# Kernel tuning notes

Hardware: AMD Instinct MI355X
Metric: run time of the kernel (lower is better)

## Reference

```python
import jax, jax.numpy as jnp
import numpy as np

B, T, NIN = 128, 256, 16
H1 = H2 = 512
NACT = 4
SLOPE = 25.0  # snntorch FastSigmoid default slope

@jax.custom_vjp
def spike(x):
    return (x > 0).astype(x.dtype)

def _spike_fwd(x):
    return (x > 0).astype(x.dtype), x

def _spike_bwd(x, g):
    # FastSigmoid surrogate: d/dx = 1 / (slope*|x| + 1)^2
    return (g / (SLOPE * jnp.abs(x) + 1.0) ** 2,)

spike.defvjp(_spike_fwd, _spike_bwd)

def setup_inputs() -> dict:
    key = jax.random.key(0)
    ks = jax.random.split(key, 12)
    def lin(k, fan_in, shape):
        lim = 1.0 / np.sqrt(fan_in)
        return jax.random.uniform(k, shape, jnp.float32, -lim, lim)
    return {
        "batch": jax.random.uniform(ks[0], (B, T, NIN), jnp.float32, 0.0, 2.5),
        "W1": lin(ks[1], NIN, (H1, NIN)), "b1": lin(ks[2], NIN, (H1,)),
        "beta1": jax.random.uniform(ks[3], (H1,), jnp.float32),
        "thr1": jax.random.uniform(ks[4], (H1,), jnp.float32),
        "W2": lin(ks[5], H1, (H2, H1)), "b2": lin(ks[6], H1, (H2,)),
        "beta2": jax.random.uniform(ks[7], (H2,), jnp.float32),
        "thr2": jax.random.uniform(ks[8], (H2,), jnp.float32),
        "Wa": lin(ks[9], H2, (NACT, H2)), "ba": lin(ks[10], H2, (NACT,)),
        "beta_act": jnp.float32(0.95),
        "inp_min": jnp.float32(0.0),
        "inp_max": jnp.float32(2.5),
    }

def _lif_subtract(cur, mem, beta, thr):
    # snntorch Leaky: reset from PRE-update membrane, detached; subtract reset
    reset = jax.lax.stop_gradient((mem - thr > 0).astype(mem.dtype))
    mem = jnp.clip(beta, 0.0, 1.0) * mem + cur - reset * thr
    return spike(mem - thr), mem

def reference(batch, W1, b1, beta1, thr1, W2, b2, beta2, thr2, Wa, ba, beta_act, inp_min, inp_max):
    Bb = batch.shape[0]
    x_seq = jnp.swapaxes(batch, 0, 1)  # [T, B, NIN]
    mem1 = jnp.zeros((Bb, W1.shape[0]), batch.dtype)
    mem2 = jnp.zeros((Bb, W2.shape[0]), batch.dtype)
    mem_a = jnp.zeros((Bb, Wa.shape[0]), batch.dtype)

    def step(carry, x):
        mem1, mem2, mem_a = carry
        x = (x - inp_min) / (inp_max - inp_min)
        spk1, mem1 = _lif_subtract(x @ W1.T + b1, mem1, beta1, thr1)
        spk2, mem2 = _lif_subtract(spk1 @ W2.T + b2, mem2, beta2, thr2)
        act = spk2 @ Wa.T + ba
        # action_lif: reset_mechanism='none', beta=0.95 learnable
        mem_a = jnp.clip(beta_act, 0.0, 1.0) * mem_a + act
        return (mem1, mem2, mem_a), mem_a.reshape(-1)  # torch: mem_act.reshape((1,-1))

    _, vals = jax.lax.scan(step, (mem1, mem2, mem_a), x_seq)
    # torch.stack(values, dim=1) of (1, B*NACT) tensors -> (1, T, B*NACT)
    return vals[None, :, :]
```

## Files before the change

### kernel.cpp

```cpp
#include <hip/hip_runtime.h>
#include <stdint.h>

typedef __attribute__((ext_vector_type(8))) short short8;
typedef __attribute__((ext_vector_type(4))) float f32x4;

#define T_STEPS 256
#define BATCH   128

#define LDS_BARRIER() asm volatile("s_waitcnt lgkmcnt(0)\n\ts_barrier" ::: "memory")

static __device__ inline unsigned short f2bf(float f) {
    unsigned int u = __float_as_uint(f);
    unsigned int r = u + 0x7FFFu + ((u >> 16) & 1u);
    return (unsigned short)(r >> 16);
}
static __device__ inline unsigned pack_hi16(unsigned a, unsigned b) {
    return __builtin_amdgcn_perm(b, a, 0x07060302u);
}
static __device__ inline void gload_lds16(const unsigned short* g, unsigned short* l) {
    __builtin_amdgcn_global_load_lds(
        (const __attribute__((address_space(1))) unsigned int*)(const void*)g,
        (__attribute__((address_space(3))) unsigned int*)(void*)l,
        16, 0, 0);
}

__global__ __launch_bounds__(256) void k_prep(
    const float* __restrict__ W2, const float* __restrict__ W1,
    const float* __restrict__ b1, const float* __restrict__ thr1,
    const float* __restrict__ imin_p, const float* __restrict__ imax_p,
    const float* __restrict__ batch,
    unsigned short* __restrict__ W2hi, unsigned short* __restrict__ W2lo,
    unsigned short* __restrict__ W1rows, float* __restrict__ b1s,
    unsigned short* __restrict__ Xf)
{
    int blk = blockIdx.x, tid = threadIdx.x;
    if (blk < 256) {
        int gid = blk * 256 + tid;
        f32x4 wv = *(const f32x4*)(W2 + (size_t)gid * 4);
        unsigned short hi[4], lo[4];
#pragma unroll
        for (int e = 0; e < 4; ++e) {
            float wf = wv[e];
            unsigned short h = f2bf(wf);
            float hf = __uint_as_float(((unsigned int)h) << 16);
            hi[e] = h;
            lo[e] = f2bf(wf - hf);
        }
        uint2 ph, pl;
        ph.x = (unsigned)hi[0] | ((unsigned)hi[1] << 16);
        ph.y = (unsigned)hi[2] | ((unsigned)hi[3] << 16);
        pl.x = (unsigned)lo[0] | ((unsigned)lo[1] << 16);
        pl.y = (unsigned)lo[2] | ((unsigned)lo[3] << 16);
        *(uint2*)(W2hi + (size_t)gid * 4) = ph;
        *(uint2*)(W2lo + (size_t)gid * 4) = pl;
    } else if (blk < 258) {
        int h = (blk - 256) * 256 + tid;
        float wsc = 1.0f / thr1[h];
        unsigned short row[64];
#pragma unroll
        for (int k = 0; k < 16; ++k) {
            float wv = W1[h * 16 + k] * wsc;
            unsigned a = __float_as_uint(wv) & 0xFFFF0000u;
            float r1 = wv - __uint_as_float(a);
            unsigned m = __float_as_uint(r1) & 0xFFFF0000u;
            float r2 = r1 - __uint_as_float(m);
            unsigned l = __float_as_uint(r2) & 0xFFFF0000u;
            row[k]      = (unsigned short)(a >> 16);
            row[16 + k] = (unsigned short)(m >> 16);
            row[32 + k] = (unsigned short)(l >> 16);
            row[48 + k] = 0;
        }
        b1s[h] = b1[h] * wsc;
        uint4* dst = (uint4*)(W1rows + (size_t)h * 64);
#pragma unroll
        for (int i = 0; i < 8; ++i) dst[i] = ((uint4*)row)[i];
    } else {
        int gid    = (blk - 258) * 256 + tid;
        int lane32 = gid & 31;
        int btile  = (gid >> 5) & 7;
        int t      = gid >> 8;
        int q1 = lane32 >> 4, m15 = lane32 & 15;
        int b  = btile * 16 + m15;
        float imin = imin_p[0];
        float isc  = 1.0f / (imax_p[0] - imin);
        const float* xp = batch + ((size_t)b * T_STEPS + t) * 16 + q1 * 8;
        unsigned uh[8], um[8], ul[8];
#pragma unroll
        for (int j = 0; j < 8; ++j) {
            float xv = (xp[j] - imin) * isc;
            unsigned a = __float_as_uint(xv) & 0xFFFF0000u;
            float r1 = xv - __uint_as_float(a);
            unsigned m = __float_as_uint(r1) & 0xFFFF0000u;
            float r2 = r1 - __uint_as_float(m);
            unsigned l = __float_as_uint(r2) & 0xFFFF0000u;
            uh[j] = a; um[j] = m; ul[j] = l;
        }
        uint4 XH, XM, XL;
        XH.x = pack_hi16(uh[0], uh[1]); XH.y = pack_hi16(uh[2], uh[3]);
        XH.z = pack_hi16(uh[4], uh[5]); XH.w = pack_hi16(uh[6], uh[7]);
        XM.x = pack_hi16(um[0], um[1]); XM.y = pack_hi16(um[2], um[3]);
        XM.z = pack_hi16(um[4], um[5]); XM.w = pack_hi16(um[6], um[7]);
        XL.x = pack_hi16(ul[0], ul[1]); XL.y = pack_hi16(ul[2], ul[3]);
        XL.z = pack_hi16(ul[4], ul[5]); XL.w = pack_hi16(ul[6], ul[7]);
        unsigned short* dst = Xf + ((size_t)t * 8 + btile) * 1024 + lane32 * 8;
        *(uint4*)(dst +   0) = XH;
        *(uint4*)(dst + 256) = XM;
        *(uint4*)(dst + 512) = XL;
    }
}

union XF { uint4 u; short8 s; };

__global__ __launch_bounds__(1024, 4) void k_main(
    const unsigned short* __restrict__ Xf,
    const unsigned short* __restrict__ W2hi, const unsigned short* __restrict__ W2lo,
    const unsigned short* __restrict__ W1rows, const float* __restrict__ b1s,
    const float* __restrict__ beta1, const float* __restrict__ b2,
    const float* __restrict__ beta2, const float* __restrict__ thr2,
    unsigned short* __restrict__ spkbits)
{
    __shared__ unsigned short Aw[8192];
    __shared__ float Cbuf[2][4096];
    __shared__ unsigned short Xs[4096];

    int tid  = threadIdx.x;
    int lane = tid & 63;
    int w    = tid >> 6;
    int q = lane >> 4, m15 = lane & 15;
    int btile = blockIdx.x & 7;
    int slice = blockIdx.x >> 3;

    short8 A1[2], A2[2], A3[2];
#pragma unroll
    for (int c = 0; c < 2; ++c) {
        const unsigned short* rp = W1rows + (size_t)(w * 32 + c * 16 + m15) * 64;
        A1[c] = *(const short8*)(rp + q * 8);
        A2[c] = *(const short8*)(rp + q * 8 + (q >> 1) * 16);
        A3[c] = *(const short8*)(rp + 16 + q * 8);
    }
    int jg = slice * 16 + m15;
    short8 bhi = *(const short8*)(W2hi + (size_t)jg * 512 + w * 32 + q * 8);
    short8 blo = *(const short8*)(W2lo + (size_t)jg * 512 + w * 32 + q * 8);

    f32x4 b14[2], bet1[2];
#pragma unroll
    for (int c = 0; c < 2; ++c) {
        int h0 = w * 32 + c * 16 + q * 4;
        b14[c] = *(const f32x4*)(b1s + h0);
        f32x4 bb = *(const f32x4*)(beta1 + h0);
#pragma unroll
        for (int r = 0; r < 4; ++r) bet1[c][r] = fminf(fmaxf(bb[r], 0.0f), 1.0f);
    }
    float m1[8], spk1f[8];
#pragma unroll
    for (int i = 0; i < 8; ++i) { m1[i] = 0.0f; spk1f[i] = 0.0f; }

    float beta2r = fminf(fmaxf(beta2[jg], 0.0f), 1.0f);
    float thr2r  = thr2[jg];
    float nthr2  = -thr2r;
    float b2r    = b2[jg];
    float m2 = 0.0f, spk2f = 0.0f;

    const unsigned short* xgbase = Xf + (size_t)btile * 1024 + (size_t)lane * 8;
    int l31x8 = (lane & 31) * 8;
    int o1 = l31x8;
    int o2 = l31x8 + 256;
    int o3 = l31x8 + (lane < 32 ? 512 : 0);
    int o4 = l31x8 + (lane < 32 ? 512 : 256);

    unsigned short* myAw = Aw + w * 512;
    int wr0 = (0 * 2 + (q >> 1)) * 128 + (m15 ^ (q >> 1)) * 8 + (q & 1) * 4;
    int wr1 = (1 * 2 + (q >> 1)) * 128 + (m15 ^ (q >> 1)) * 8 + (q & 1) * 4;
    int rdo = (q * 16 + (m15 ^ (q & 1))) * 8;

    if (w == 15) {
        gload_lds16(xgbase,              Xs);
        gload_lds16(xgbase + 512,        Xs + 512);
        gload_lds16(xgbase + 8192,       Xs + 1024);
        gload_lds16(xgbase + 8192 + 512, Xs + 1536);
        asm volatile("s_waitcnt vmcnt(0)" ::: "memory");
    }
    __syncthreads();

    XF xc[4], xn[4];
    {
        const unsigned short* s = Xs;
        xc[0].u = *(const uint4*)(s + o1);
        xc[1].u = *(const uint4*)(s + o2);
        xc[2].u = *(const uint4*)(s + o3);
        xc[3].u = *(const uint4*)(s + o4);
    }

    auto body = [&](int ts, XF* xcur, XF* xnx) __attribute__((always_inline)) {
        int buf = ts & 1;
        if (w == 15) {
            int t2 = (ts + 2 < T_STEPS) ? ts + 2 : T_STEPS - 1;
            const unsigned short* g = xgbase + (size_t)t2 * 8192;
            unsigned short* l = Xs + (((ts + 2) & 3) << 10);
            gload_lds16(g,       l);
            gload_lds16(g + 512, l + 512);
        }
        {
            const unsigned short* s = Xs + (((ts + 1) & 3) << 10);
            xnx[0].u = *(const uint4*)(s + o1);
            xnx[1].u = *(const uint4*)(s + o2);
            xnx[2].u = *(const uint4*)(s + o3);
            xnx[3].u = *(const uint4*)(s + o4);
        }

        f32x4 D[2];
#pragma unroll
        for (int c = 0; c < 2; ++c) {
            D[c] = __builtin_amdgcn_mfma_f32_16x16x32_bf16(A1[c], xcur[0].s, b14[c], 0, 0, 0);
            D[c] = __builtin_amdgcn_mfma_f32_16x16x32_bf16(A1[c], xcur[1].s, D[c], 0, 0, 0);
            D[c] = __builtin_amdgcn_mfma_f32_16x16x32_bf16(A2[c], xcur[2].s, D[c], 0, 0, 0);
            D[c] = __builtin_amdgcn_mfma_f32_16x16x32_bf16(A3[c], xcur[3].s, D[c], 0, 0, 0);
        }
#pragma unroll
        for (int i = 0; i < 8; ++i) {
            int c = i >> 2, r = i & 3;
            float mv = fmaf(bet1[c][r], m1[i], D[c][r]);
            mv -= spk1f[i];
            bool sp = mv > 1.0f;
            m1[i] = mv;
            spk1f[i] = sp ? 1.0f : 0.0f;
        }
        {
            uint2 pk0, pk1;
            pk0.x = pack_hi16(__float_as_uint(spk1f[0]), __float_as_uint(spk1f[1]));
            pk0.y = pack_hi16(__float_as_uint(spk1f[2]), __float_as_uint(spk1f[3]));
            pk1.x = pack_hi16(__float_as_uint(spk1f[4]), __float_as_uint(spk1f[5]));
            pk1.y = pack_hi16(__float_as_uint(spk1f[6]), __float_as_uint(spk1f[7]));
            *(uint2*)(myAw + wr0) = pk0;
            *(uint2*)(myAw + wr1) = pk1;
        }
        union { uint4 u; short8 s; } af;
        af.u = *(uint4*)(myAw + rdo);
        f32x4 C2 = { 0.f, 0.f, 0.f, 0.f };
        C2 = __builtin_amdgcn_mfma_f32_16x16x32_bf16(af.s, bhi, C2, 0, 0, 0);
        C2 = __builtin_amdgcn_mfma_f32_16x16x32_bf16(af.s, blo, C2, 0, 0, 0);
#pragma unroll
        for (int r = 0; r < 4; ++r)
            Cbuf[buf][r * 1024 + w * 64 + lane] = C2[r];
        if (w == 15) asm volatile("s_waitcnt vmcnt(0)" ::: "memory");
        LDS_BARRIER();
        if (w < 4) {
            float cur2 = b2r;
#pragma unroll
            for (int wp = 0; wp < 16; ++wp) cur2 += Cbuf[buf][w * 1024 + wp * 64 + lane];
            m2 = fmaf(beta2r, m2, cur2);
            m2 = fmaf(spk2f, nthr2, m2);
            bool sp2 = m2 > thr2r;
            spk2f = sp2 ? 1.0f : 0.0f;
            unsigned long long mask = __ballot(sp2);
            if (lane < 4) {
                unsigned short v = (unsigned short)(mask >> (lane * 16));
                spkbits[((size_t)ts * BATCH + btile * 16 + lane * 4 + w) * 32 + slice] = v;
            }
        }
    };

#pragma unroll 1
    for (int ts = 0; ts < T_STEPS; ts += 2) {
        body(ts, xc, xn);
        body(ts + 1, xn, xc);
    }
}

__global__ __launch_bounds__(256) void k_act(
    const unsigned short* __restrict__ spkbits,
    const float* __restrict__ Wa, const float* __restrict__ ba,
    const float* __restrict__ beta_act_p, float* __restrict__ out)
{
    __shared__ f32x4 waT[512];
    __shared__ f32x4 sc[256];
    int tid = threadIdx.x;
    int b   = blockIdx.x;

    for (int j = tid; j < 512; j += 256) {
        f32x4 v = { Wa[j], Wa[512 + j], Wa[1024 + j], Wa[1536 + j] };
        waT[j] = v;
    }
    float bact = fminf(fmaxf(beta_act_p[0], 0.0f), 1.0f);
    f32x4 acc = { ba[0], ba[1], ba[2], ba[3] };
    __syncthreads();

    const unsigned short* sp = spkbits + ((size_t)tid * BATCH + b) * 32;
    unsigned int wbuf[16];
#pragma unroll
    for (int r = 0; r < 4; ++r) {
        uint4 v = *(const uint4*)(sp + r * 8);
        wbuf[r*4+0] = v.x; wbuf[r*4+1] = v.y; wbuf[r*4+2] = v.z; wbuf[r*4+3] = v.w;
    }
    for (int s = 0; s < 32; ++s) {
        unsigned int wd = (wbuf[s >> 1] >> ((s & 1) * 16)) & 0xFFFFu;
#pragma unroll
        for (int i = 0; i < 16; ++i) {
            float sel = ((wd >> i) & 1u) ? 1.0f : 0.0f;
            f32x4 wv = waT[s * 16 + i];
            acc[0] = fmaf(sel, wv[0], acc[0]);
            acc[1] = fmaf(sel, wv[1], acc[1]);
            acc[2] = fmaf(sel, wv[2], acc[2]);
            acc[3] = fmaf(sel, wv[3], acc[3]);
        }
    }
    sc[tid] = acc;
    __syncthreads();
    float bd = bact;
    for (int d = 1; d < 256; d <<= 1) {
        f32x4 cv = sc[tid];
        f32x4 pv = { 0.f, 0.f, 0.f, 0.f };
        if (tid >= d) pv = sc[tid - d];
        __syncthreads();
        cv[0] = fmaf(bd, pv[0], cv[0]);
        cv[1] = fmaf(bd, pv[1], cv[1]);
        cv[2] = fmaf(bd, pv[2], cv[2]);
        cv[3] = fmaf(bd, pv[3], cv[3]);
        sc[tid] = cv;
        __syncthreads();
        bd *= bd;
    }
    f32x4 res = sc[tid];
    *(f32x4*)(out + (size_t)tid * 512 + b * 4) = res;
}

extern "C" void kernel_launch(void* const* d_in, const int* in_sizes, int n_in,
                              void* d_out, int out_size, void* d_ws, size_t ws_size,
                              hipStream_t stream)
{
    const float* batch    = (const float*)d_in[0];
    const float* W1       = (const float*)d_in[1];
    const float* b1       = (const float*)d_in[2];
    const float* beta1    = (const float*)d_in[3];
    const float* thr1     = (const float*)d_in[4];
    const float* W2       = (const float*)d_in[5];
    const float* b2       = (const float*)d_in[6];
    const float* beta2    = (const float*)d_in[7];
    const float* thr2     = (const float*)d_in[8];
    const float* Wa       = (const float*)d_in[9];
    const float* ba       = (const float*)d_in[10];
    const float* beta_act = (const float*)d_in[11];
    const float* inp_min  = (const float*)d_in[12];
    const float* inp_max  = (const float*)d_in[13];
    float* out            = (float*)d_out;

    char* ws = (char*)d_ws;
    unsigned short* W2hi    = (unsigned short*)ws;
    unsigned short* W2lo    = (unsigned short*)(ws + (512u << 10));
    unsigned short* W1rows  = (unsigned short*)(ws + (1u << 20));
    float*          b1s     = (float*)(ws + (1u << 20) + (64u << 10));
    unsigned short* Xf      = (unsigned short*)(ws + (2u << 20));
    unsigned short* spkbits = (unsigned short*)(ws + (10u << 20));

    hipLaunchKernelGGL(k_prep, dim3(514), dim3(256), 0, stream,
                       W2, W1, b1, thr1, inp_min, inp_max, batch,
                       W2hi, W2lo, W1rows, b1s, Xf);
    hipLaunchKernelGGL(k_main, dim3(256), dim3(1024), 0, stream,
                       Xf, W2hi, W2lo, W1rows, b1s, beta1, b2, beta2, thr2, spkbits);
    hipLaunchKernelGGL(k_act, dim3(128), dim3(256), 0, stream, spkbits, Wa, ba, beta_act, out);
}
```

Before: 289.0 us.

## Halve per-step barriers by batching layer-2 reductions and split action scan

```diff
diff --git a/kernel.cpp b/kernel.cpp
--- a/kernel.cpp
+++ b/kernel.cpp
@@ -120,8 +120,8 @@
     unsigned short* __restrict__ spkbits)
 {
     __shared__ unsigned short Aw[8192];
-    __shared__ float Cbuf[2][4096];
-    __shared__ unsigned short Xs[4096];
+    __shared__ float Cbuf[4][4096];
+    __shared__ unsigned short Xs[8192];
 
     int tid  = threadIdx.x;
     int lane = tid & 63;
@@ -174,10 +174,11 @@
     int rdo = (q * 16 + (m15 ^ (q & 1))) * 8;
 
     if (w == 15) {
-        gload_lds16(xgbase,              Xs);
-        gload_lds16(xgbase + 512,        Xs + 512);
-        gload_lds16(xgbase + 8192,       Xs + 1024);
-        gload_lds16(xgbase + 8192 + 512, Xs + 1536);
+#pragma unroll
+        for (int s = 0; s < 4; ++s) {
+            gload_lds16(xgbase + (size_t)s * 8192,       Xs + s * 1024);
+            gload_lds16(xgbase + (size_t)s * 8192 + 512, Xs + s * 1024 + 512);
+        }
         asm volatile("s_waitcnt vmcnt(0)" ::: "memory");
     }
     __syncthreads();
@@ -191,23 +192,41 @@
         xc[3].u = *(const uint4*)(s + o4);
     }
 
-    auto body = [&](int ts, XF* xcur, XF* xnx) __attribute__((always_inline)) {
-        int buf = ts & 1;
-        if (w == 15) {
-            int t2 = (ts + 2 < T_STEPS) ? ts + 2 : T_STEPS - 1;
-            const unsigned short* g = xgbase + (size_t)t2 * 8192;
-            unsigned short* l = Xs + (((ts + 2) & 3) << 10);
-            gload_lds16(g,       l);
-            gload_lds16(g + 512, l + 512);
+    auto reduce_one = [&](int slot, int step) __attribute__((always_inline)) {
+        float cur2 = b2r;
+#pragma unroll
+        for (int wp = 0; wp < 16; ++wp) cur2 += Cbuf[slot][w * 1024 + wp * 64 + lane];
+        m2 = fmaf(beta2r, m2, cur2);
+        m2 = fmaf(spk2f, nthr2, m2);
+        bool sp2 = m2 > thr2r;
+        spk2f = sp2 ? 1.0f : 0.0f;
+        unsigned long long mask = __ballot(sp2);
+        if (lane < 4) {
+            unsigned short v = (unsigned short)(mask >> (lane * 16));
+            spkbits[((size_t)step * BATCH + btile * 16 + lane * 4 + w) * 32 + slice] = v;
+        }
+    };
+
+    auto gbody = [&](int ts, int k, XF* xcur, XF* xnx) __attribute__((always_inline)) {
+        if (((k & 1) == 0) && w == 15) {
+            int ta = ts + k + 4; if (ta > T_STEPS - 1) ta = T_STEPS - 1;
+            int tb = ts + k + 5; if (tb > T_STEPS - 1) tb = T_STEPS - 1;
+            const unsigned short* ga = xgbase + (size_t)ta * 8192;
+            const unsigned short* gb = xgbase + (size_t)tb * 8192;
+            unsigned short* la = Xs + ((k + 4) & 7) * 1024;
+            unsigned short* lb = Xs + ((k + 5) & 7) * 1024;
+            gload_lds16(ga,       la);
+            gload_lds16(ga + 512, la + 512);
+            gload_lds16(gb,       lb);
+            gload_lds16(gb + 512, lb + 512);
         }
         {
-            const unsigned short* s = Xs + (((ts + 1) & 3) << 10);
-            xnx[0].u = *(const uint4*)(s + o1);
-            xnx[1].u = *(const uint4*)(s + o2);
-            xnx[2].u = *(const uint4*)(s + o3);
-            xnx[3].u = *(const uint4*)(s + o4);
-        }
-
+            const unsigned short* sx = Xs + ((k + 1) & 7) * 1024;
+            xnx[0].u = *(const uint4*)(sx + o1);
+            xnx[1].u = *(const uint4*)(sx + o2);
+            xnx[2].u = *(const uint4*)(sx + o3);
+            xnx[3].u = *(const uint4*)(sx + o4);
+        }
         f32x4 D[2];
 #pragma unroll
         for (int c = 0; c < 2; ++c) {
@@ -239,89 +258,141 @@
         f32x4 C2 = { 0.f, 0.f, 0.f, 0.f };
         C2 = __builtin_amdgcn_mfma_f32_16x16x32_bf16(af.s, bhi, C2, 0, 0, 0);
         C2 = __builtin_amdgcn_mfma_f32_16x16x32_bf16(af.s, blo, C2, 0, 0, 0);
+        float* cb = Cbuf[k & 3];
 #pragma unroll
         for (int r = 0; r < 4; ++r)
-            Cbuf[buf][r * 1024 + w * 64 + lane] = C2[r];
-        if (w == 15) asm volatile("s_waitcnt vmcnt(0)" ::: "memory");
-        LDS_BARRIER();
-        if (w < 4) {
-            float cur2 = b2r;
-#pragma unroll
-            for (int wp = 0; wp < 16; ++wp) cur2 += Cbuf[buf][w * 1024 + wp * 64 + lane];
-            m2 = fmaf(beta2r, m2, cur2);
-            m2 = fmaf(spk2f, nthr2, m2);
-            bool sp2 = m2 > thr2r;
-            spk2f = sp2 ? 1.0f : 0.0f;
-            unsigned long long mask = __ballot(sp2);
-            if (lane < 4) {
-                unsigned short v = (unsigned short)(mask >> (lane * 16));
-                spkbits[((size_t)ts * BATCH + btile * 16 + lane * 4 + w) * 32 + slice] = v;
+            cb[r * 1024 + w * 64 + lane] = C2[r];
+        if (k & 1) {
+            if (w == 15) asm volatile("s_waitcnt vmcnt(0)" ::: "memory");
+            LDS_BARRIER();
+        }
+    };
+
+#pragma unroll 1
+    for (int ts = 0; ts < T_STEPS; ts += 8) {
+#pragma unroll
+        for (int kk = 0; kk < 4; ++kk) {
+            int k = kk * 2;
+            if (w < 4 && (ts + k >= 2)) {
+                reduce_one((k + 2) & 3, ts + k - 2);
+                reduce_one((k + 3) & 3, ts + k - 1);
             }
-        }
-    };
-
-#pragma unroll 1
-    for (int ts = 0; ts < T_STEPS; ts += 2) {
-        body(ts, xc, xn);
-        body(ts + 1, xn, xc);
-    }
-}
-
-__global__ __launch_bounds__(256) void k_act(
+            gbody(ts, k,     xc, xn);
+            gbody(ts, k + 1, xn, xc);
+        }
+    }
+    if (w < 4) {
+        reduce_one(2, T_STEPS - 2);
+        reduce_one(3, T_STEPS - 1);
+    }
+}
+
+__global__ __launch_bounds__(512) void k_act(
     const unsigned short* __restrict__ spkbits,
     const float* __restrict__ Wa, const float* __restrict__ ba,
+    const float* __restrict__ beta_act_p, float* __restrict__ out,
+    f32x4* __restrict__ Lws, f32x4* __restrict__ Cws)
+{
+    __shared__ f32x4 waT[512];
+    __shared__ f32x4 part[512];
+    __shared__ f32x4 sc[128];
+    int tid = threadIdx.x;
+    int b   = blockIdx.x & 127;
+    int c   = blockIdx.x >> 7;
+    int tl  = tid & 127;
+    int s   = tid >> 7;
+    int t   = c * 128 + tl;
+
+    {
+        f32x4 v = { Wa[tid], Wa[512 + tid], Wa[1024 + tid], Wa[1536 + tid] };
+        waT[tid] = v;
+    }
+    float bact = fminf(fmaxf(beta_act_p[0], 0.0f), 1.0f);
+    f32x4 acc;
+    if (s == 0) { acc[0] = ba[0]; acc[1] = ba[1]; acc[2] = ba[2]; acc[3] = ba[3]; }
+    else        { acc[0] = 0.f;   acc[1] = 0.f;   acc[2] = 0.f;   acc[3] = 0.f;   }
+    __syncthreads();
+
+    const unsigned short* sp = spkbits + ((size_t)t * BATCH + b) * 32 + s * 8;
+    uint4 v = *(const uint4*)sp;
+    unsigned int wbuf[4] = { v.x, v.y, v.z, v.w };
+#pragma unroll
+    for (int ww = 0; ww < 4; ++ww) {
+#pragma unroll
+        for (int half = 0; half < 2; ++half) {
+            unsigned int wd = (wbuf[ww] >> (half * 16)) & 0xFFFFu;
+            int seg = s * 8 + ww * 2 + half;
+#pragma unroll
+            for (int i = 0; i < 16; ++i) {
+                float sel = ((wd >> i) & 1u) ? 1.0f : 0.0f;
+                f32x4 wv = waT[seg * 16 + i];
+                acc[0] = fmaf(sel, wv[0], acc[0]);
+                acc[1] = fmaf(sel, wv[1], acc[1]);
+                acc[2] = fmaf(sel, wv[2], acc[2]);
+                acc[3] = fmaf(sel, wv[3], acc[3]);
+            }
+        }
+    }
+    part[tid] = acc;
+    __syncthreads();
+    if (tid < 128) {
+        f32x4 a0 = part[tid], a1 = part[tid + 128], a2 = part[tid + 256], a3 = part[tid + 384];
+        f32x4 sum;
+        sum[0] = ((a0[0] + a1[0]) + a2[0]) + a3[0];
+        sum[1] = ((a0[1] + a1[1]) + a2[1]) + a3[1];
+        sum[2] = ((a0[2] + a1[2]) + a2[2]) + a3[2];
+        sum[3] = ((a0[3] + a1[3]) + a2[3]) + a3[3];
+        sc[tid] = sum;
+    }
+    __syncthreads();
+    float bd = bact;
+    for (int d = 1; d < 128; d <<= 1) {
+        f32x4 cv = { 0.f, 0.f, 0.f, 0.f }, pv = { 0.f, 0.f, 0.f, 0.f };
+        if (tid < 128) {
+            cv = sc[tid];
+            if (tid >= d) pv = sc[tid - d];
+        }
+        __syncthreads();
+        if (tid < 128) {
+            cv[0] = fmaf(bd, pv[0], cv[0]);
+            cv[1] = fmaf(bd, pv[1], cv[1]);
+            cv[2] = fmaf(bd, pv[2], cv[2]);
+            cv[3] = fmaf(bd, pv[3], cv[3]);
+            sc[tid] = cv;
+        }
+        __syncthreads();
+        bd *= bd;
+    }
+    if (tid < 128) {
+        f32x4 res = sc[tid];
+        if (c == 0) {
+            *(f32x4*)(out + (size_t)t * 512 + b * 4) = res;
+            if (tl == 127) Cws[b] = res;
+        } else {
+            Lws[b * 128 + tl] = res;
+        }
+    }
+}
+
+__global__ __launch_bounds__(128) void k_act2(
+    const f32x4* __restrict__ Lws, const f32x4* __restrict__ Cws,
     const float* __restrict__ beta_act_p, float* __restrict__ out)
 {
-    __shared__ f32x4 waT[512];
-    __shared__ f32x4 sc[256];
-    int tid = threadIdx.x;
-    int b   = blockIdx.x;
-
-    for (int j = tid; j < 512; j += 256) {
-        f32x4 v = { Wa[j], Wa[512 + j], Wa[1024 + j], Wa[1536 + j] };
-        waT[j] = v;
-    }
+    int tl = threadIdx.x;
+    int b  = blockIdx.x;
     float bact = fminf(fmaxf(beta_act_p[0], 0.0f), 1.0f);
-    f32x4 acc = { ba[0], ba[1], ba[2], ba[3] };
-    __syncthreads();
-
-    const unsigned short* sp = spkbits + ((size_t)tid * BATCH + b) * 32;
-    unsigned int wbuf[16];
-#pragma unroll
-    for (int r = 0; r < 4; ++r) {
-        uint4 v = *(const uint4*)(sp + r * 8);
-        wbuf[r*4+0] = v.x; wbuf[r*4+1] = v.y; wbuf[r*4+2] = v.z; wbuf[r*4+3] = v.w;
-    }
-    for (int s = 0; s < 32; ++s) {
-        unsigned int wd = (wbuf[s >> 1] >> ((s & 1) * 16)) & 0xFFFFu;
-#pragma unroll
-        for (int i = 0; i < 16; ++i) {
-            float sel = ((wd >> i) & 1u) ? 1.0f : 0.0f;
-            f32x4 wv = waT[s * 16 + i];
-            acc[0] = fmaf(sel, wv[0], acc[0]);
-            acc[1] = fmaf(sel, wv[1], acc[1]);
-            acc[2] = fmaf(sel, wv[2], acc[2]);
-            acc[3] = fmaf(sel, wv[3], acc[3]);
-        }
-    }
-    sc[tid] = acc;
-    __syncthreads();
-    float bd = bact;
-    for (int d = 1; d < 256; d <<= 1) {
-        f32x4 cv = sc[tid];
-        f32x4 pv = { 0.f, 0.f, 0.f, 0.f };
-        if (tid >= d) pv = sc[tid - d];
-        __syncthreads();
-        cv[0] = fmaf(bd, pv[0], cv[0]);
-        cv[1] = fmaf(bd, pv[1], cv[1]);
-        cv[2] = fmaf(bd, pv[2], cv[2]);
-        cv[3] = fmaf(bd, pv[3], cv[3]);
-        sc[tid] = cv;
-        __syncthreads();
-        bd *= bd;
-    }
-    f32x4 res = sc[tid];
-    *(f32x4*)(out + (size_t)tid * 512 + b * 4) = res;
+    float p = 1.0f, base = bact;
+    int e = tl + 1;
+#pragma unroll
+    for (int i = 0; i < 8; ++i) { if (e & 1) p *= base; base *= base; e >>= 1; }
+    f32x4 L = Lws[b * 128 + tl];
+    f32x4 C = Cws[b];
+    f32x4 r;
+    r[0] = fmaf(p, C[0], L[0]);
+    r[1] = fmaf(p, C[1], L[1]);
+    r[2] = fmaf(p, C[2], L[2]);
+    r[3] = fmaf(p, C[3], L[3]);
+    *(f32x4*)(out + (size_t)(128 + tl) * 512 + b * 4) = r;
 }
 
 extern "C" void kernel_launch(void* const* d_in, const int* in_sizes, int n_in,
@@ -350,6 +421,8 @@
     unsigned short* W1rows  = (unsigned short*)(ws + (1u << 20));
     float*          b1s     = (float*)(ws + (1u << 20) + (64u << 10));
     unsigned short* Xf      = (unsigned short*)(ws + (2u << 20));
+    f32x4*          Lws     = (f32x4*)(ws + (6u << 20));
+    f32x4*          Cws     = (f32x4*)(ws + (6u << 20) + (256u << 10));
     unsigned short* spkbits = (unsigned short*)(ws + (10u << 20));
 
     hipLaunchKernelGGL(k_prep, dim3(514), dim3(256), 0, stream,
@@ -357,5 +430,7 @@
                        W2hi, W2lo, W1rows, b1s, Xf);
     hipLaunchKernelGGL(k_main, dim3(256), dim3(1024), 0, stream,
                        Xf, W2hi, W2lo, W1rows, b1s, beta1, b2, beta2, thr2, spkbits);
-    hipLaunchKernelGGL(k_act, dim3(128), dim3(256), 0, stream, spkbits, Wa, ba, beta_act, out);
-}
+    hipLaunchKernelGGL(k_act, dim3(256), dim3(512), 0, stream,
+                       spkbits, Wa, ba, beta_act, out, Lws, Cws);
+    hipLaunchKernelGGL(k_act2, dim3(128), dim3(128), 0, stream, Lws, Cws, beta_act, out);
+}
```

New measurement: 258.7 us. 1.12x faster.
